# Performance work log

Hardware: AMD Instinct MI355X
Metric: run time of the kernel (lower is better)

## Reference

```python
import jax, jax.numpy as jnp
import numpy as np

B, S, H = 4, 1024, 1024
NH, HD = 16, 64
SCALE = 1.0 / np.sqrt(HD)
VERB_BIAS, ROOT_BIAS, SUFFIX_BIAS = 2.0, 1.5, 1.2
BIG = np.float32(1e9)


def setup_inputs() -> dict:
    key = jax.random.key(0)
    ks = jax.random.split(key, 10)
    inp = {
        "hidden_states": jax.random.normal(ks[0], (B, S, H), dtype=jnp.float32),
        "morpho_types": jax.random.randint(ks[1], (B, S), 0, 5, dtype=jnp.int32),
        # torch Linear: y = x @ W.T + b; store W already transposed as [in, out]
        "Wq": jax.random.normal(ks[2], (H, H), dtype=jnp.float32) * 0.02,
        "bq": jnp.zeros((H,), dtype=jnp.float32),
        "Wk": jax.random.normal(ks[3], (H, H), dtype=jnp.float32) * 0.02,
        "bk": jnp.zeros((H,), dtype=jnp.float32),
        "Wv": jax.random.normal(ks[4], (H, H), dtype=jnp.float32) * 0.02,
        "bv": jnp.zeros((H,), dtype=jnp.float32),
        "Wo": jax.random.normal(ks[5], (H, H), dtype=jnp.float32) * 0.02,
        "bo": jnp.zeros((H,), dtype=jnp.float32),
    }
    return inp


def _morpho_bias(morpho_types):
    """Vectorized equivalent of _create_morpho_bias_mask. Returns [B, S, S]
    (the torch version broadcasts the same bias over all heads)."""
    is_verb = morpho_types == 2                      # [B, S]
    pos = jnp.arange(S)
    dist = jnp.abs(pos[:, None] - pos[None, :])      # [S, S]
    # mask non-verb columns with a huge distance; argmin ties -> smallest j,
    # matching torch's argmin over ascending verb_positions
    dist_m = jnp.where(is_verb[:, None, :], dist[None], BIG)  # [B, S, S]
    nearest = jnp.argmin(dist_m, axis=-1)            # [B, S]
    has_verb = jnp.any(is_verb, axis=-1)             # [B]
    verb_term = VERB_BIAS * jax.nn.one_hot(nearest, S, dtype=jnp.float32)
    verb_term = verb_term * has_verb[:, None, None].astype(jnp.float32)
    col_bias = (ROOT_BIAS * 0.5) * (morpho_types == 0).astype(jnp.float32) \
             + (SUFFIX_BIAS * 0.3) * (morpho_types == 1).astype(jnp.float32)  # [B, S]
    return verb_term + col_bias[:, None, :]          # [B, S, S]


def reference(hidden_states, morpho_types, Wq, bq, Wk, bk, Wv, bv, Wo, bo):
    def proj(W, b):
        y = hidden_states @ W + b                    # [B, S, H]
        return y.reshape(B, S, NH, HD).transpose(0, 2, 1, 3)  # [B, NH, S, HD]

    q = proj(Wq, bq)
    k = proj(Wk, bk)
    v = proj(Wv, bv)

    scores = jnp.einsum('bhqd,bhkd->bhqk', q, k) * SCALE   # [B, NH, S, S]
    scores = scores + _morpho_bias(morpho_types)[:, None]  # broadcast heads

    attn = jax.nn.softmax(scores, axis=-1)
    out = jnp.einsum('bhqk,bhkd->bhqd', attn, v)           # [B, NH, S, HD]
    out = out.transpose(0, 2, 1, 3).reshape(B, S, H)
    return out @ Wo + bo
```

## Files before the change

### kernel.cpp

```cpp
#include <hip/hip_runtime.h>


#define QSCALE 0.18033688011112042f
#define CB0    1.0820212806667225f
#define CB1    0.5193702147200268f
#define VERB2  2.8853900817779268f

typedef float  f32x4   __attribute__((ext_vector_type(4)));
typedef short  s16x8   __attribute__((ext_vector_type(8)));
typedef unsigned short u16x4 __attribute__((ext_vector_type(4)));
typedef unsigned short u16x8 __attribute__((ext_vector_type(8)));

#if __has_builtin(__builtin_amdgcn_exp2f)
#define EXP2F(x) __builtin_amdgcn_exp2f(x)
#else
#define EXP2F(x) exp2f(x)
#endif

__device__ __forceinline__ unsigned short f2bf(float f) {
  union { float f; unsigned u; } a; a.f = f;
  unsigned r = a.u + 0x7fffu + ((a.u >> 16) & 1u);
  return (unsigned short)(r >> 16);
}

__device__ __forceinline__ void async16(const void* g, void* l) {
  __builtin_amdgcn_global_load_lds(
      (const __attribute__((address_space(1))) unsigned int*)g,
      (__attribute__((address_space(3))) unsigned int*)l, 16, 0, 0);
}

__global__ __launch_bounds__(256) void k_prep(
    const float* __restrict__ hs, unsigned short* __restrict__ hsb,
    const float* __restrict__ Wq, const float* __restrict__ Wk,
    const float* __restrict__ Wv, const float* __restrict__ Wo,
    unsigned short* __restrict__ Wt, const int* __restrict__ mt,
    float* __restrict__ colbias, int* __restrict__ nearest) {
  __shared__ float t[64 * 68];
  int bx = blockIdx.x, tid = threadIdx.x;
  if (bx < 2048) {
    int i = (bx * 256 + tid) * 8;
    float4 v0 = *(const float4*)(hs + i);
    float4 v1 = *(const float4*)(hs + i + 4);
    u16x8 o;
    o[0] = f2bf(v0.x); o[1] = f2bf(v0.y); o[2] = f2bf(v0.z); o[3] = f2bf(v0.w);
    o[4] = f2bf(v1.x); o[5] = f2bf(v1.y); o[6] = f2bf(v1.z); o[7] = f2bf(v1.w);
    *(u16x8*)(hsb + i) = o;
  } else if (bx < 3072) {
    int w = (bx - 2048) >> 8, tt = (bx - 2048) & 255;
    const float* W = (w == 0) ? Wq : (w == 1) ? Wk : (w == 2) ? Wv : Wo;
    unsigned short* Wd = Wt + (size_t)w * 1048576;
    int n0 = (tt & 15) * 64, k0 = (tt >> 4) * 64;
    int r = tid >> 2, c0 = (tid & 3) * 16;
    const float* src = &W[(k0 + r) * 1024 + n0 + c0];
    float4 a0 = *(const float4*)(src + 0);
    float4 a1 = *(const float4*)(src + 4);
    float4 a2 = *(const float4*)(src + 8);
    float4 a3 = *(const float4*)(src + 12);
    *(float4*)&t[r * 68 + c0 + 0]  = a0;
    *(float4*)&t[r * 68 + c0 + 4]  = a1;
    *(float4*)&t[r * 68 + c0 + 8]  = a2;
    *(float4*)&t[r * 68 + c0 + 12] = a3;
    __syncthreads();
    u16x8 o0, o1;
#pragma unroll
    for (int j = 0; j < 8; j++) {
      o0[j] = f2bf(t[(c0 + j) * 68 + r]);
      o1[j] = f2bf(t[(c0 + 8 + j) * 68 + r]);
    }
    *(u16x8*)&Wd[(n0 + r) * 1024 + k0 + c0]     = o0;
    *(u16x8*)&Wd[(n0 + r) * 1024 + k0 + c0 + 8] = o1;
  } else {
    int i = bx - 3072;
    int b = i >> 2;
    int* sm = (int*)t;
    for (int j = tid; j < 1024; j += 256) sm[j] = mt[b * 1024 + j];
    __syncthreads();
    int q = (i & 3) * 256 + tid;
    int best = 1 << 30, bj = -1;
    for (int j = 0; j < 1024; ++j) {
      int d = (q > j) ? (q - j) : (j - q);
      int dd = (sm[j] == 2) ? d : (1 << 30);
      if (dd < best) { best = dd; bj = j; }
    }
    nearest[b * 1024 + q] = bj;
    int m = sm[q];
    colbias[b * 1024 + q] = CB0 * (m == 0) + CB1 * (m == 1);
  }
}

template <int MODE>
__global__ __launch_bounds__(256) void k_gemm(
    const unsigned short* __restrict__ A,
    const unsigned short* __restrict__ WtBase,
    const float* __restrict__ bias0, const float* __restrict__ bias1,
    const float* __restrict__ bias2,
    unsigned short* __restrict__ outB, unsigned short* __restrict__ outV,
    float* __restrict__ outF) {
  constexpr int TM = (MODE == 0) ? 128 : 64;
  constexpr int NI = (MODE == 0) ? 4 : 2;
  constexpr int RA = TM / 4;
  __shared__ unsigned short As[TM * 64];
  __shared__ unsigned short Bs[128 * 64];
  int tid = threadIdx.x, wid = tid >> 6, lane = tid & 63;
  int c = lane & 15, quad = lane >> 4;
  int m0, wsel, n0;
  const unsigned short* Bt;
  const float* bias;
  if (MODE == 0) {
    wsel = blockIdx.x >> 3;
    n0 = (blockIdx.x & 7) * 128;
    m0 = blockIdx.y * 128;
    Bt = WtBase + wsel * 1048576;
    bias = (wsel == 0) ? bias0 : ((wsel == 1) ? bias1 : bias2);
  } else {
    wsel = 0;
    n0 = blockIdx.x * 128;
    m0 = blockIdx.y * 64;
    Bt = WtBase; bias = bias0;
  }
  int wm = (wid >> 1) * (16 * NI), wn = (wid & 1) * 64;
  int lr = lane >> 3, lc = lane & 7;
  int gcol = ((lc ^ lr) << 3);
  const unsigned short* ga = A  + (size_t)(m0 + wid * RA + lr) * 1024 + gcol;
  const unsigned short* gb = Bt + (size_t)(n0 + wid * 32 + lr) * 1024 + gcol;
  unsigned short* lA = &As[(wid * RA) * 64];
  unsigned short* lB = &Bs[(wid * 32) * 64];

  f32x4 acc[NI][4];
#pragma unroll
  for (int i = 0; i < NI; i++)
#pragma unroll
    for (int j = 0; j < 4; j++) acc[i][j] = (f32x4){0.f, 0.f, 0.f, 0.f};

  bool sw = (MODE == 1) || (wsel != 2);

  for (int k0 = 0; k0 < 1024; k0 += 64) {
#pragma unroll
    for (int i = 0; i < RA / 8; i++) async16(ga + i * 8 * 1024 + k0, lA + i * 8 * 64);
#pragma unroll
    for (int j = 0; j < 4; j++)      async16(gb + j * 8 * 1024 + k0, lB + j * 8 * 64);
    __syncthreads();
#pragma unroll
    for (int ks = 0; ks < 2; ks++) {
      s16x8 af[NI], bf[4];
#pragma unroll
      for (int i = 0; i < NI; i++)
        af[i] = *(const s16x8*)&As[(wm + i * 16 + c) * 64 + (((ks * 4 + quad) ^ (c & 7)) << 3)];
#pragma unroll
      for (int j = 0; j < 4; j++)
        bf[j] = *(const s16x8*)&Bs[(wn + j * 16 + c) * 64 + (((ks * 4 + quad) ^ (c & 7)) << 3)];
      if (sw) {
#pragma unroll
        for (int i = 0; i < NI; i++)
#pragma unroll
          for (int j = 0; j < 4; j++)
            acc[i][j] = __builtin_amdgcn_mfma_f32_16x16x32_bf16(bf[j], af[i], acc[i][j], 0, 0, 0);
      } else {
#pragma unroll
        for (int i = 0; i < NI; i++)
#pragma unroll
          for (int j = 0; j < 4; j++)
            acc[i][j] = __builtin_amdgcn_mfma_f32_16x16x32_bf16(af[i], bf[j], acc[i][j], 0, 0, 0);
      }
    }
    __syncthreads();
  }

  if (MODE == 1) {
#pragma unroll
    for (int j = 0; j < 4; j++) {
      int colb = n0 + wn + j * 16 + quad * 4;
      f32x4 bvv = *(const f32x4*)&bias[colb];
#pragma unroll
      for (int i = 0; i < NI; i++) {
        int s_tok = m0 + wm + i * 16 + c;
        f32x4 v = acc[i][j] + bvv;
        *(f32x4*)&outF[(size_t)s_tok * 1024 + colb] = v;
      }
    }
  } else if (wsel == 2) {
#pragma unroll
    for (int j = 0; j < 4; j++) {
      int col = n0 + wn + j * 16 + c;
      float bv = bias[col];
      int h = col >> 6, d = col & 63;
#pragma unroll
      for (int i = 0; i < NI; i++) {
        int row = m0 + wm + i * 16 + quad * 4;
        int bb = row >> 10, s = row & 1023;
        u16x4 pk;
#pragma unroll
        for (int r = 0; r < 4; r++) pk[r] = f2bf(acc[i][j][r] + bv);
        *(u16x4*)&outV[(size_t)(((bb * 16 + h) * 64 + d)) * 1024 + s] = pk;
      }
    }
  } else {
    float sc = (wsel == 0) ? QSCALE : 1.0f;
#pragma unroll
    for (int j = 0; j < 4; j++) {
      int colb = n0 + wn + j * 16 + quad * 4;
      f32x4 bvv = *(const f32x4*)&bias[colb];
      int h = colb >> 6, d0 = colb & 63;
#pragma unroll
      for (int i = 0; i < NI; i++) {
        int s_tok = m0 + wm + i * 16 + c;
        int bb = s_tok >> 10, s = s_tok & 1023;
        u16x4 pk;
#pragma unroll
        for (int r = 0; r < 4; r++) pk[r] = f2bf((acc[i][j][r] + bvv[r]) * sc);
        *(u16x4*)&outB[(size_t)wsel * 4194304 + (((bb * 16 + h) * 1024 + s) * 64) + d0] = pk;
      }
    }
  }
}

__global__ __launch_bounds__(256) void k_attn(
    const unsigned short* __restrict__ Q, const unsigned short* __restrict__ K,
    const unsigned short* __restrict__ Vt, const float* __restrict__ colbias,
    const int* __restrict__ nearest, unsigned short* __restrict__ AO) {
  __shared__ unsigned short Ks[2][64 * 64];
  __shared__ unsigned short Vs[2][64 * 64];
  __shared__ unsigned short Ps[4][16 * 64];
  __shared__ float Cb[1024];
  int tid = threadIdx.x, wid = tid >> 6, lane = tid & 63;
  int c = lane & 15, quad = lane >> 4;
  int bh = blockIdx.x, qt = blockIdx.y;
  int b = bh >> 4, head = bh & 15;
  int q0 = qt * 64, wq = wid * 16;
  const unsigned short* Qg = Q  + (size_t)(bh * 1024 + q0 + wq) * 64;
  const unsigned short* Kg = K  + (size_t)bh * 1024 * 64;
  const unsigned short* Vg = Vt + (size_t)bh * 64 * 1024;

  *(float4*)&Cb[tid * 4] = *(const float4*)&colbias[b * 1024 + tid * 4];

  s16x8 qf[2];
#pragma unroll
  for (int ks = 0; ks < 2; ks++)
    qf[ks] = *(const s16x8*)&Qg[c * 64 + ks * 32 + quad * 8];

  int nq = nearest[b * 1024 + q0 + wq + c];

  f32x4 o[4];
#pragma unroll
  for (int j = 0; j < 4; j++) o[j] = (f32x4){0.f, 0.f, 0.f, 0.f};
  float lrun = 0.f;

  int srow = tid >> 3;
  int swz8 = (((tid & 7) ^ (srow & 7)) << 3);
  int scol8 = (tid & 7) * 8;
  const int cs = c & 7;

  u16x8 kr[2], vr[2];
#pragma unroll
  for (int it = 0; it < 2; ++it) {
    int r2 = it * 32 + srow;
    kr[it] = *(const u16x8*)&Kg[r2 * 64 + scol8];
    vr[it] = *(const u16x8*)&Vg[r2 * 1024 + scol8];
  }
#pragma unroll
  for (int it = 0; it < 2; ++it) {
    int r2 = it * 32 + srow;
    *(u16x8*)&Ks[0][r2 * 64 + swz8] = kr[it];
    *(u16x8*)&Vs[0][r2 * 64 + swz8] = vr[it];
  }
#pragma unroll
  for (int it = 0; it < 2; ++it) {
    int r2 = it * 32 + srow;
    kr[it] = *(const u16x8*)&Kg[(64 + r2) * 64 + scol8];
    vr[it] = *(const u16x8*)&Vg[r2 * 1024 + 64 + scol8];
  }
  __syncthreads();

  for (int kc = 0; kc < 16; ++kc) {
    int cur = kc & 1;
    if (kc < 15) {
#pragma unroll
      for (int it = 0; it < 2; ++it) {
        int r2 = it * 32 + srow;
        *(u16x8*)&Ks[cur ^ 1][r2 * 64 + swz8] = kr[it];
        *(u16x8*)&Vs[cur ^ 1][r2 * 64 + swz8] = vr[it];
      }
    }
    if (kc < 14) {
#pragma unroll
      for (int it = 0; it < 2; ++it) {
        int r2 = it * 32 + srow;
        kr[it] = *(const u16x8*)&Kg[((kc + 2) * 64 + r2) * 64 + scol8];
        vr[it] = *(const u16x8*)&Vg[r2 * 1024 + (kc + 2) * 64 + scol8];
      }
    }

    f32x4 st[4];
#pragma unroll
    for (int mt = 0; mt < 4; mt++) st[mt] = (f32x4){0.f, 0.f, 0.f, 0.f};
#pragma unroll
    for (int mt = 0; mt < 4; mt++)
#pragma unroll
      for (int ks = 0; ks < 2; ks++) {
        s16x8 a = *(const s16x8*)&Ks[cur][(mt * 16 + c) * 64 + (((ks * 4 + quad) ^ cs) << 3)];
        st[mt] = __builtin_amdgcn_mfma_f32_16x16x32_bf16(a, qf[ks], st[mt], 0, 0, 0);
      }

    if (__any((nq >> 6) == kc)) {
#pragma unroll
      for (int mt = 0; mt < 4; mt++)
#pragma unroll
        for (int r = 0; r < 4; r++)
          if (kc * 64 + mt * 16 + quad * 4 + r == nq) st[mt][r] += VERB2;
    }

#pragma unroll
    for (int mt = 0; mt < 4; mt++) {
      f32x4 cb = *(const f32x4*)&Cb[kc * 64 + mt * 16 + quad * 4];
      float e0 = EXP2F(st[mt][0] + cb[0]);
      float e1 = EXP2F(st[mt][1] + cb[1]);
      float e2 = EXP2F(st[mt][2] + cb[2]);
      float e3 = EXP2F(st[mt][3] + cb[3]);
      unsigned p01 = __builtin_amdgcn_perm(__float_as_uint(e1), __float_as_uint(e0), 0x07060302u);
      unsigned p23 = __builtin_amdgcn_perm(__float_as_uint(e3), __float_as_uint(e2), 0x07060302u);
      lrun += __uint_as_float(p01 << 16) + __uint_as_float(p01 & 0xffff0000u)
            + __uint_as_float(p23 << 16) + __uint_as_float(p23 & 0xffff0000u);
      uint2 pk; pk.x = p01; pk.y = p23;
      int chs = (2 * mt + (quad >> 1)) ^ cs;
      *(uint2*)&Ps[wid][c * 64 + chs * 8 + (quad & 1) * 4] = pk;
    }
    __asm__ volatile("s_waitcnt lgkmcnt(0)" ::: "memory");

#pragma unroll
    for (int ks = 0; ks < 2; ks++) {
      s16x8 pa = *(const s16x8*)&Ps[wid][c * 64 + (((ks * 4 + quad) ^ cs) << 3)];
#pragma unroll
      for (int ntd = 0; ntd < 4; ntd++) {
        s16x8 vb = *(const s16x8*)&Vs[cur][(ntd * 16 + c) * 64 + (((ks * 4 + quad) ^ cs) << 3)];
        o[ntd] = __builtin_amdgcn_mfma_f32_16x16x32_bf16(vb, pa, o[ntd], 0, 0, 0);
      }
    }
    __syncthreads();
  }

  lrun += __shfl_xor(lrun, 16, 64);
  lrun += __shfl_xor(lrun, 32, 64);
  float linv = 1.0f / lrun;
  size_t row = (size_t)(b * 1024 + q0 + wq + c);
#pragma unroll
  for (int ntd = 0; ntd < 4; ntd++) {
    int d0 = ntd * 16 + quad * 4;
    u16x4 pk;
#pragma unroll
    for (int r = 0; r < 4; r++) pk[r] = f2bf(o[ntd][r] * linv);
    *(u16x4*)&AO[row * 1024 + head * 64 + d0] = pk;
  }
}

extern "C" void kernel_launch(void* const* d_in, const int* in_sizes, int n_in,
                              void* d_out, int out_size, void* d_ws, size_t ws_size,
                              hipStream_t stream) {
  const float* hs     = (const float*)d_in[0];
  const int*   morpho = (const int*)d_in[1];
  const float* Wq = (const float*)d_in[2];
  const float* bq = (const float*)d_in[3];
  const float* Wk = (const float*)d_in[4];
  const float* bk = (const float*)d_in[5];
  const float* Wv = (const float*)d_in[6];
  const float* bv = (const float*)d_in[7];
  const float* Wo = (const float*)d_in[8];
  const float* bo = (const float*)d_in[9];
  float* out = (float*)d_out;

  char* ws = (char*)d_ws;
  unsigned short* hsb = (unsigned short*)(ws);
  unsigned short* Wt  = (unsigned short*)(ws + (8u << 20));
  unsigned short* Qb  = (unsigned short*)(ws + (16u << 20));
  unsigned short* Kb  = (unsigned short*)(ws + (24u << 20));
  unsigned short* Vtb = (unsigned short*)(ws + (40u << 20));
  float* colbias      = (float*)(ws + (48u << 20));
  int*   nearestp     = (int*)(ws + (48u << 20) + (16u << 10));
  unsigned short* AO  = hsb;

  k_prep<<<3088, 256, 0, stream>>>(hs, hsb, Wq, Wk, Wv, Wo, Wt, morpho,
                                   colbias, nearestp);
  k_gemm<0><<<dim3(24, 32), 256, 0, stream>>>(hsb, Wt, bq, bk, bv, Qb, Vtb, nullptr);
  k_attn<<<dim3(64, 16), 256, 0, stream>>>(Qb, Kb, Vtb, colbias, nearestp, AO);
  k_gemm<1><<<dim3(8, 64), 256, 0, stream>>>(AO, Wt + 3 * 1048576, bo, nullptr, nullptr,
                                             nullptr, nullptr, out);
  (void)in_sizes; (void)n_in; (void)out_size; (void)ws_size; (void)Kb;
}
```

Before: 211.8 us.

## Fuse all stages into one persistent kernel with atomic grid barriers

Replaces the four kernel launches (prep, QKV GEMM, attention, output GEMM) with a single persistent kernel of 768 blocks. Blocks pull work units from atomic counters in the workspace and wait at software grid barriers (spin loops with sleep) between stages. All stages share one statically sized shared-memory buffer. This removes per-launch overhead and the gaps between kernels, but adds barrier spin cost. It also relies on all 768 blocks being co-resident, and combining every stage's code in one kernel may raise register pressure or limit occupancy.

```diff
diff --git a/kernel.cpp b/kernel.cpp
--- a/kernel.cpp
+++ b/kernel.cpp
@@ -29,14 +29,15 @@
       (__attribute__((address_space(3))) unsigned int*)l, 16, 0, 0);
 }
 
-__global__ __launch_bounds__(256) void k_prep(
+
+__device__ __forceinline__ void prep_unit(
+    int bx, int tid, unsigned char* SM,
     const float* __restrict__ hs, unsigned short* __restrict__ hsb,
     const float* __restrict__ Wq, const float* __restrict__ Wk,
     const float* __restrict__ Wv, const float* __restrict__ Wo,
     unsigned short* __restrict__ Wt, const int* __restrict__ mt,
     float* __restrict__ colbias, int* __restrict__ nearest) {
-  __shared__ float t[64 * 68];
-  int bx = blockIdx.x, tid = threadIdx.x;
+  float* t = (float*)SM;
   if (bx < 2048) {
     int i = (bx * 256 + tid) * 8;
     float4 v0 = *(const float4*)(hs + i);
@@ -69,6 +70,7 @@
     }
     *(u16x8*)&Wd[(n0 + r) * 1024 + k0 + c0]     = o0;
     *(u16x8*)&Wd[(n0 + r) * 1024 + k0 + c0 + 8] = o1;
+    __syncthreads();
   } else {
     int i = bx - 3072;
     int b = i >> 2;
@@ -85,11 +87,13 @@
     nearest[b * 1024 + q] = bj;
     int m = sm[q];
     colbias[b * 1024 + q] = CB0 * (m == 0) + CB1 * (m == 1);
+    __syncthreads();
   }
 }
 
 template <int MODE>
-__global__ __launch_bounds__(256) void k_gemm(
+__device__ __forceinline__ void gemm_unit(
+    int bx, int by, int tid, unsigned char* SM,
     const unsigned short* __restrict__ A,
     const unsigned short* __restrict__ WtBase,
     const float* __restrict__ bias0, const float* __restrict__ bias1,
@@ -99,23 +103,23 @@
   constexpr int TM = (MODE == 0) ? 128 : 64;
   constexpr int NI = (MODE == 0) ? 4 : 2;
   constexpr int RA = TM / 4;
-  __shared__ unsigned short As[TM * 64];
-  __shared__ unsigned short Bs[128 * 64];
-  int tid = threadIdx.x, wid = tid >> 6, lane = tid & 63;
+  unsigned short* As = (unsigned short*)SM;
+  unsigned short* Bs = (unsigned short*)SM + TM * 64;
+  int wid = tid >> 6, lane = tid & 63;
   int c = lane & 15, quad = lane >> 4;
   int m0, wsel, n0;
   const unsigned short* Bt;
   const float* bias;
   if (MODE == 0) {
-    wsel = blockIdx.x >> 3;
-    n0 = (blockIdx.x & 7) * 128;
-    m0 = blockIdx.y * 128;
+    wsel = bx >> 3;
+    n0 = (bx & 7) * 128;
+    m0 = by * 128;
     Bt = WtBase + wsel * 1048576;
     bias = (wsel == 0) ? bias0 : ((wsel == 1) ? bias1 : bias2);
   } else {
     wsel = 0;
-    n0 = blockIdx.x * 128;
-    m0 = blockIdx.y * 64;
+    n0 = bx * 128;
+    m0 = by * 64;
     Bt = WtBase; bias = bias0;
   }
   int wm = (wid >> 1) * (16 * NI), wn = (wid & 1) * 64;
@@ -214,17 +218,18 @@
   }
 }
 
-__global__ __launch_bounds__(256) void k_attn(
+__device__ __forceinline__ void attn_unit(
+    int u, int tid, unsigned char* SM,
     const unsigned short* __restrict__ Q, const unsigned short* __restrict__ K,
     const unsigned short* __restrict__ Vt, const float* __restrict__ colbias,
     const int* __restrict__ nearest, unsigned short* __restrict__ AO) {
-  __shared__ unsigned short Ks[2][64 * 64];
-  __shared__ unsigned short Vs[2][64 * 64];
-  __shared__ unsigned short Ps[4][16 * 64];
-  __shared__ float Cb[1024];
-  int tid = threadIdx.x, wid = tid >> 6, lane = tid & 63;
+  unsigned short* KsB = (unsigned short*)SM;
+  unsigned short* VsB = (unsigned short*)(SM + 16384);
+  unsigned short* Ps  = (unsigned short*)(SM + 32768);
+  float* Cb           = (float*)(SM + 40960);
+  int wid = tid >> 6, lane = tid & 63;
   int c = lane & 15, quad = lane >> 4;
-  int bh = blockIdx.x, qt = blockIdx.y;
+  int bh = u >> 4, qt = u & 15;
   int b = bh >> 4, head = bh & 15;
   int q0 = qt * 64, wq = wid * 16;
   const unsigned short* Qg = Q  + (size_t)(bh * 1024 + q0 + wq) * 64;
@@ -260,8 +265,8 @@
 #pragma unroll
   for (int it = 0; it < 2; ++it) {
     int r2 = it * 32 + srow;
-    *(u16x8*)&Ks[0][r2 * 64 + swz8] = kr[it];
-    *(u16x8*)&Vs[0][r2 * 64 + swz8] = vr[it];
+    *(u16x8*)&KsB[r2 * 64 + swz8] = kr[it];
+    *(u16x8*)&VsB[r2 * 64 + swz8] = vr[it];
   }
 #pragma unroll
   for (int it = 0; it < 2; ++it) {
@@ -273,12 +278,16 @@
 
   for (int kc = 0; kc < 16; ++kc) {
     int cur = kc & 1;
+    unsigned short* Kc = KsB + cur * 4096;
+    unsigned short* Vc = VsB + cur * 4096;
+    unsigned short* Kn = KsB + (cur ^ 1) * 4096;
+    unsigned short* Vn = VsB + (cur ^ 1) * 4096;
     if (kc < 15) {
 #pragma unroll
       for (int it = 0; it < 2; ++it) {
         int r2 = it * 32 + srow;
-        *(u16x8*)&Ks[cur ^ 1][r2 * 64 + swz8] = kr[it];
-        *(u16x8*)&Vs[cur ^ 1][r2 * 64 + swz8] = vr[it];
+        *(u16x8*)&Kn[r2 * 64 + swz8] = kr[it];
+        *(u16x8*)&Vn[r2 * 64 + swz8] = vr[it];
       }
     }
     if (kc < 14) {
@@ -297,7 +306,7 @@
     for (int mt = 0; mt < 4; mt++)
 #pragma unroll
       for (int ks = 0; ks < 2; ks++) {
-        s16x8 a = *(const s16x8*)&Ks[cur][(mt * 16 + c) * 64 + (((ks * 4 + quad) ^ cs) << 3)];
+        s16x8 a = *(const s16x8*)&Kc[(mt * 16 + c) * 64 + (((ks * 4 + quad) ^ cs) << 3)];
         st[mt] = __builtin_amdgcn_mfma_f32_16x16x32_bf16(a, qf[ks], st[mt], 0, 0, 0);
       }
 
@@ -322,16 +331,16 @@
             + __uint_as_float(p23 << 16) + __uint_as_float(p23 & 0xffff0000u);
       uint2 pk; pk.x = p01; pk.y = p23;
       int chs = (2 * mt + (quad >> 1)) ^ cs;
-      *(uint2*)&Ps[wid][c * 64 + chs * 8 + (quad & 1) * 4] = pk;
+      *(uint2*)&Ps[wid * 1024 + c * 64 + chs * 8 + (quad & 1) * 4] = pk;
     }
     __asm__ volatile("s_waitcnt lgkmcnt(0)" ::: "memory");
 
 #pragma unroll
     for (int ks = 0; ks < 2; ks++) {
-      s16x8 pa = *(const s16x8*)&Ps[wid][c * 64 + (((ks * 4 + quad) ^ cs) << 3)];
+      s16x8 pa = *(const s16x8*)&Ps[wid * 1024 + c * 64 + (((ks * 4 + quad) ^ cs) << 3)];
 #pragma unroll
       for (int ntd = 0; ntd < 4; ntd++) {
-        s16x8 vb = *(const s16x8*)&Vs[cur][(ntd * 16 + c) * 64 + (((ks * 4 + quad) ^ cs) << 3)];
+        s16x8 vb = *(const s16x8*)&Vc[(ntd * 16 + c) * 64 + (((ks * 4 + quad) ^ cs) << 3)];
         o[ntd] = __builtin_amdgcn_mfma_f32_16x16x32_bf16(vb, pa, o[ntd], 0, 0, 0);
       }
     }
@@ -349,6 +358,111 @@
 #pragma unroll
     for (int r = 0; r < 4; r++) pk[r] = f2bf(o[ntd][r] * linv);
     *(u16x4*)&AO[row * 1024 + head * 64 + d0] = pk;
+  }
+}
+
+__global__ __launch_bounds__(256, 3) void k_fused(
+    const float* __restrict__ hs, const int* __restrict__ morpho,
+    const float* __restrict__ Wq, const float* __restrict__ Wk,
+    const float* __restrict__ Wv, const float* __restrict__ Wo,
+    const float* __restrict__ bq, const float* __restrict__ bk,
+    const float* __restrict__ bv, const float* __restrict__ bo,
+    float* __restrict__ out, char* __restrict__ ws) {
+  __shared__ __align__(16) unsigned char SM[45056];
+  __shared__ int s_u;
+  unsigned short* hsb = (unsigned short*)ws;
+  unsigned short* Wt  = (unsigned short*)(ws + (8u  << 20));
+  unsigned short* Qb  = (unsigned short*)(ws + (16u << 20));
+  unsigned short* Kb  = (unsigned short*)(ws + (24u << 20));
+  unsigned short* Vtb = (unsigned short*)(ws + (40u << 20));
+  float* colbias      = (float*)(ws + (48u << 20));
+  int*   nearestp     = (int*)(ws + (48u << 20) + (16u << 10));
+  int*   ctr          = (int*)(ws + (32u << 20));
+  unsigned short* AO  = hsb;
+  int tid = threadIdx.x;
+
+  {
+    int my = 0;
+    for (;;) {
+      if (tid == 0) s_u = atomicAdd(&ctr[0], 1);
+      __syncthreads();
+      int u = s_u;
+      __syncthreads();
+      if (u >= 3088) break;
+      prep_unit(u, tid, SM, hs, hsb, Wq, Wk, Wv, Wo, Wt, morpho, colbias, nearestp);
+      ++my;
+    }
+    __syncthreads();
+    if (tid == 0) {
+      __threadfence();
+      if (my) atomicAdd(&ctr[1], my);
+      int spins = 0;
+      while (atomicAdd(&ctr[1], 0) < 3088 && spins < 5000000) {
+        __builtin_amdgcn_s_sleep(2); ++spins;
+      }
+    }
+    __syncthreads();
+    __threadfence();
+  }
+
+  {
+    int my = 0;
+    for (;;) {
+      if (tid == 0) s_u = atomicAdd(&ctr[2], 1);
+      __syncthreads();
+      int u = s_u;
+      __syncthreads();
+      if (u >= 768) break;
+      gemm_unit<0>(u % 24, u / 24, tid, SM, hsb, Wt, bq, bk, bv, Qb, Vtb, nullptr);
+      ++my;
+    }
+    __syncthreads();
+    if (tid == 0) {
+      __threadfence();
+      if (my) atomicAdd(&ctr[3], my);
+      int spins = 0;
+      while (atomicAdd(&ctr[3], 0) < 768 && spins < 5000000) {
+        __builtin_amdgcn_s_sleep(2); ++spins;
+      }
+    }
+    __syncthreads();
+    __threadfence();
+  }
+
+  {
+    int my = 0;
+    for (;;) {
+      if (tid == 0) s_u = atomicAdd(&ctr[4], 1);
+      __syncthreads();
+      int u = s_u;
+      __syncthreads();
+      if (u >= 1024) break;
+      attn_unit(u, tid, SM, Qb, Kb, Vtb, colbias, nearestp, AO);
+      ++my;
+    }
+    __syncthreads();
+    if (tid == 0) {
+      __threadfence();
+      if (my) atomicAdd(&ctr[5], my);
+      int spins = 0;
+      while (atomicAdd(&ctr[5], 0) < 1024 && spins < 5000000) {
+        __builtin_amdgcn_s_sleep(2); ++spins;
+      }
+    }
+    __syncthreads();
+    __threadfence();
+  }
+
+  {
+    for (;;) {
+      if (tid == 0) s_u = atomicAdd(&ctr[6], 1);
+      __syncthreads();
+      int u = s_u;
+      __syncthreads();
+      if (u >= 512) break;
+      gemm_unit<1>(u & 7, u >> 3, tid, SM, AO, Wt + 3 * 1048576, bo,
+                   nullptr, nullptr, nullptr, nullptr, out);
+    }
   }
 }
 
@@ -366,22 +480,11 @@
   const float* Wo = (const float*)d_in[8];
   const float* bo = (const float*)d_in[9];
   float* out = (float*)d_out;
-
   char* ws = (char*)d_ws;
-  unsigned short* hsb = (unsigned short*)(ws);
-  unsigned short* Wt  = (unsigned short*)(ws + (8u << 20));
-  unsigned short* Qb  = (unsigned short*)(ws + (16u << 20));
-  unsigned short* Kb  = (unsigned short*)(ws + (24u << 20));
-  unsigned short* Vtb = (unsigned short*)(ws + (40u << 20));
-  float* colbias      = (float*)(ws + (48u << 20));
-  int*   nearestp     = (int*)(ws + (48u << 20) + (16u << 10));
-  unsigned short* AO  = hsb;
-
-  k_prep<<<3088, 256, 0, stream>>>(hs, hsb, Wq, Wk, Wv, Wo, Wt, morpho,
-                                   colbias, nearestp);
-  k_gemm<0><<<dim3(24, 32), 256, 0, stream>>>(hsb, Wt, bq, bk, bv, Qb, Vtb, nullptr);
-  k_attn<<<dim3(64, 16), 256, 0, stream>>>(Qb, Kb, Vtb, colbias, nearestp, AO);
-  k_gemm<1><<<dim3(8, 64), 256, 0, stream>>>(AO, Wt + 3 * 1048576, bo, nullptr, nullptr,
-                                             nullptr, nullptr, out);
-  (void)in_sizes; (void)n_in; (void)out_size; (void)ws_size; (void)Kb;
-}
+
+  hipMemsetAsync(ws + (32u << 20), 0, 64, stream);
+
+  k_fused<<<768, 256, 0, stream>>>(hs, morpho, Wq, Wk, Wv, Wo,
+                                   bq, bk, bv, bo, out, ws);
+  (void)in_sizes; (void)n_in; (void)out_size; (void)ws_size;
+}
```

Result: slower. 768.9 us (+263.0%).
